# Kernel tuning notes

Hardware: AMD Instinct MI355X
Metric: run time of the kernel (lower is better)

The kernel has to match this reference:

```python
import jax, jax.numpy as jnp
import numpy as np

DECAY = 0.99   # LIF membrane decay
INH = 1.625    # lateral inhibition strength (mode='max')


def setup_inputs() -> dict:
    key = jax.random.key(0)
    kx, kw = jax.random.split(key)
    B, Cin, Cout = 8192, 4096, 1024
    x = (jax.random.uniform(kx, (B, Cin)) < 0.2).astype(jnp.float32)
    # weights, then normweight(): clamp to [0,1] and scale each row so row-max == 0.1
    W = jax.random.uniform(kw, (Cout, Cin), dtype=jnp.float32)
    W = W / (W.max(axis=1, keepdims=True) / 0.1)
    return {"x": x, "W": W, "time_window": 10}


def reference(x, W, time_window):
    # current through the bias-free linear layer; constant across timesteps
    i = x @ W.T                                   # (B, Cout)
    # adaptive threshold init: threshold = 3 * max over batch (thre_init branch)
    thr = 3.0 * i.max(axis=0)                     # (Cout,)
    imax = i.max(axis=1, keepdims=True)           # (B, 1), for mode='max' inhibition
    C = i.shape[1]

    def step(mem, _):
        mem = mem * DECAY + i                     # LIF integration
        s = (mem > thr).astype(i.dtype)           # threshold fire
        mem = mem * (1.0 - s)                     # hard reset at all spikers
        row = s.max(axis=1, keepdims=True)        # (B,1) 1 if any neuron in row spiked
        # winner-take-all k=1: keep a single spiking neuron per row (first/argmax)
        wta = jax.nn.one_hot(jnp.argmax(s, axis=1), C, dtype=i.dtype) * row
        # lateral inhibition: subtract inh * max-current from losers in rows that spiked
        mem = mem - INH * imax * (row - wta)
        return mem, wta

    mem0 = jnp.zeros_like(i)
    _, wtas = jax.lax.scan(step, mem0, None, length=time_window)
    return wtas.sum(axis=0)                       # accumulated spikes (B, Cout)
```

## Files before the change

kernel.cpp:

```cpp
#include <hip/hip_runtime.h>
#include <cstdint>

#define B_DIM 8192
#define CIN   4096
#define COUT  1024

constexpr double W_SCALE   = 83230720.0;
constexpr int    QMAX      = 8323072;
constexpr double INV_SCALE = 0.1 / 8323072.0;

using i32x4 = __attribute__((ext_vector_type(4))) int;

__device__ __forceinline__ void async_copy16(void* lds, const void* g) {
    auto l = (__attribute__((address_space(3))) void*)(uintptr_t)(lds);
    auto p = (const __attribute__((address_space(1))) void*)(uintptr_t)(g);
    __builtin_amdgcn_global_load_lds(p, l, 16, 0, 0);
}

__global__ void prep_x(const float* __restrict__ x, int8_t* __restrict__ Ai) {
    const int idx = blockIdx.x * 256 + threadIdx.x;
    const float4* xp = (const float4*)x + (size_t)idx * 4;
    float4 v0 = xp[0], v1 = xp[1], v2 = xp[2], v3 = xp[3];
    auto pk = [](float a, float b, float c, float d) -> int {
        return (a != 0.f ? 1 : 0) | ((b != 0.f ? 1 : 0) << 8) |
               ((c != 0.f ? 1 : 0) << 16) | ((d != 0.f ? 1 : 0) << 24);
    };
    int4 r;
    r.x = pk(v0.x, v0.y, v0.z, v0.w);
    r.y = pk(v1.x, v1.y, v1.z, v1.w);
    r.z = pk(v2.x, v2.y, v2.z, v2.w);
    r.w = pk(v3.x, v3.y, v3.z, v3.w);
    ((int4*)Ai)[idx] = r;
}

__global__ void prep_w(const float* __restrict__ W, int8_t* __restrict__ Bd,
                       unsigned long long* __restrict__ cm) {
    const int idx = blockIdx.x * 256 + threadIdx.x;
    float4 w = ((const float4*)W)[idx];
    float ws[4] = {w.x, w.y, w.z, w.w};
    char dg[3][4];
#pragma unroll
    for (int k = 0; k < 4; ++k) {
        int qv = __double2int_rn((double)ws[k] * W_SCALE);
        qv = max(0, min(QMAX, qv));
        int d0 = ((qv + 128) & 255) - 128; int tq = (qv - d0) >> 8;
        int d1 = ((tq + 128) & 255) - 128; int d2 = (tq - d1) >> 8;
        dg[0][k] = (char)d0; dg[1][k] = (char)d1; dg[2][k] = (char)d2;
    }
    const size_t off = (size_t)idx * 4;
#pragma unroll
    for (int p = 0; p < 3; ++p) {
        char4 c4; c4.x = dg[p][0]; c4.y = dg[p][1]; c4.z = dg[p][2]; c4.w = dg[p][3];
        *(char4*)(Bd + (size_t)p * COUT * CIN + off) = c4;
    }
    if (idx < COUT) cm[idx] = 0ull;
}

__device__ __forceinline__ void mma16(const i32x4 (&a)[8], const i32x4 (&b)[4],
                                      i32x4 (*accp)[2]) {
    __builtin_amdgcn_s_setprio(1);
#pragma unroll
    for (int kk = 0; kk < 2; ++kk)
#pragma unroll
        for (int mi = 0; mi < 4; ++mi)
#pragma unroll
            for (int ni = 0; ni < 2; ++ni)
                accp[mi][ni] = __builtin_amdgcn_mfma_i32_16x16x64_i8(
                    a[kk * 4 + mi], b[kk * 2 + ni], accp[mi][ni], 0, 0, 0);
    __builtin_amdgcn_s_setprio(0);
}

#define BAR()    __builtin_amdgcn_s_barrier()
#define SCHED0() __builtin_amdgcn_sched_barrier(0)
#define VMW(n)   asm volatile("s_waitcnt vmcnt(" #n ")" ::: "memory")

__global__ __launch_bounds__(256, 2) void gemm_i8(const int8_t* __restrict__ A,
                                                  const int8_t* __restrict__ Bm,
                                                  double* __restrict__ Sc,
                                                  unsigned long long* __restrict__ cm) {
    __shared__ alignas(16) int8_t lds[40960];
    const int tid  = threadIdx.x;
    const int lane = tid & 63;
    const int wave = tid >> 6;

    const int wg = (int)blockIdx.x;
    const int bn = ((wg & 7) << 1) | ((wg >> 3) & 1);
    const int bm = wg >> 4;

    const int stid   = tid >> 3;
    const int cswz16 = ((tid & 7) ^ (stid & 7)) << 4;
    const int8_t* gA = A  + (size_t)(bm * 128 + stid) * CIN + cswz16;
    const int8_t* gB = Bm + (size_t)(bn * 64  + stid) * CIN + cswz16;
    const int wv1024 = wave << 10;

#define SA_(t_) do {                                                            \
    int8_t* d_ = lds + wv1024;                                                  \
    const int8_t* s_ = gA + ((t_) << 7);                                        \
    async_copy16(d_,         s_);                                               \
    async_copy16(d_ + 4096,  s_ + (size_t)32 * CIN);                            \
    async_copy16(d_ + 8192,  s_ + (size_t)64 * CIN);                            \
    async_copy16(d_ + 12288, s_ + (size_t)96 * CIN);                            \
} while (0)
#define SB_(t_, p_) do {                                                        \
    int8_t* d_ = lds + 16384 + ((p_) << 13) + wv1024;                           \
    const int8_t* s_ = gB + (size_t)(p_) * COUT * CIN + ((t_) << 7);            \
    async_copy16(d_,        s_);                                                \
    async_copy16(d_ + 4096, s_ + (size_t)32 * CIN);                             \
} while (0)

    const int wr = wave >> 1, wc = wave & 1;
    const int fr = lane & 15;
    const int q  = lane >> 4;
    const int ck0 = (q ^ (fr & 7)) << 4;
    const int abase = (wr * 64 + fr) * 128;
    const int bbase = 16384 + (wc * 32 + fr) * 128;

    i32x4 a[8], b[4];
    i32x4 acc[3][4][2] = {};

#define LDA_() do {                                                             \
    const int8_t* p_ = lds + abase;                                             \
    _Pragma("unroll")                                                           \
    for (int kk_ = 0; kk_ < 2; ++kk_)                                           \
        _Pragma("unroll")                                                       \
        for (int mi_ = 0; mi_ < 4; ++mi_)                                       \
            a[kk_ * 4 + mi_] = *(const i32x4*)(p_ + mi_ * 2048 + (ck0 ^ (kk_ * 64))); \
} while (0)
#define LDB_(p_) do {                                                           \
    const int8_t* q_ = lds + ((p_) << 13) + bbase;                              \
    _Pragma("unroll")                                                           \
    for (int kk_ = 0; kk_ < 2; ++kk_)                                           \
        _Pragma("unroll")                                                       \
        for (int ni_ = 0; ni_ < 2; ++ni_)                                       \
            b[kk_ * 2 + ni_] = *(const i32x4*)(q_ + ni_ * 2048 + (ck0 ^ (kk_ * 64))); \
} while (0)

    SA_(0); SB_(0, 0); SB_(0, 1);
    VMW(2); BAR(); SCHED0();

#pragma unroll 1
    for (int t = 0; t < 31; ++t) {
        LDA_(); LDB_(0); SB_(t, 2);
        mma16(a, b, acc[0]); VMW(2); BAR(); SCHED0();
        LDB_(1); SA_(t + 1); SB_(t + 1, 0);
        mma16(a, b, acc[1]); VMW(6); BAR(); SCHED0();
        LDB_(2); SB_(t + 1, 1);
        mma16(a, b, acc[2]); VMW(2); BAR(); SCHED0();
    }
    LDA_(); LDB_(0); SB_(31, 2);
    mma16(a, b, acc[0]); VMW(2); BAR(); SCHED0();
    LDB_(1);
    mma16(a, b, acc[1]); VMW(0); BAR(); SCHED0();
    LDB_(2);
    mma16(a, b, acc[2]); BAR();

    const int gm0 = bm * 128 + wr * 64 + q * 4;
    const int gn0 = bn * 64 + wc * 32 + fr;
    double vmax[2] = {0.0, 0.0};
#pragma unroll
    for (int mi = 0; mi < 4; ++mi)
#pragma unroll
        for (int ni = 0; ni < 2; ++ni) {
            const int gn = gn0 + ni * 16;
#pragma unroll
            for (int reg = 0; reg < 4; ++reg) {
                const int gm = gm0 + mi * 16 + reg;
                long long isum = (long long)acc[0][mi][ni][reg]
                               + 256ll   * (long long)acc[1][mi][ni][reg]
                               + 65536ll * (long long)acc[2][mi][ni][reg];
                double v = (double)isum * INV_SCALE;
                Sc[(size_t)gm * COUT + gn] = v;
                vmax[ni] = fmax(vmax[ni], v);
            }
        }
#pragma unroll
    for (int ni = 0; ni < 2; ++ni) {
        vmax[ni] = fmax(vmax[ni], __shfl_xor(vmax[ni], 16, 64));
        vmax[ni] = fmax(vmax[ni], __shfl_xor(vmax[ni], 32, 64));
    }
    double* red = (double*)lds;
    if (lane < 16) {
#pragma unroll
        for (int ni = 0; ni < 2; ++ni)
            red[wave * 32 + ni * 16 + fr] = vmax[ni];
    }
    __syncthreads();
    if (tid < 64) {
        const int c = tid;
        double m = fmax(red[c], red[64 + c]);
        atomicMax(cm + bn * 64 + c, (unsigned long long)__double_as_longlong(m));
    }
#undef SA_
#undef SB_
#undef LDA_
#undef LDB_
}

__global__ void scan_k(const double* __restrict__ Sc, const unsigned long long* __restrict__ cm,
                       const int* __restrict__ twp, float* __restrict__ out) {
    const int lane = threadIdx.x & 63;
    const int wave = threadIdx.x >> 6;
    const int b = blockIdx.x * 4 + wave;
    const int T = *twp;
    const double* row = Sc + (size_t)b * COUT;

    double iv[16], mem[16], thr[16];
    int cnt[16];
    double imax = 0.0;
#pragma unroll
    for (int u = 0; u < 16; ++u) {
        const int j = lane + u * 64;
        iv[u]  = row[j];
        thr[u] = 3.0 * __longlong_as_double((long long)cm[j]);
        mem[u] = 0.0; cnt[u] = 0;
        imax = fmax(imax, iv[u]);
    }
#pragma unroll
    for (int d = 32; d >= 1; d >>= 1) imax = fmax(imax, __shfl_xor(imax, d, 64));
    const double h = 1.625 * imax;

    for (int t = 0; t < T; ++t) {
        int first = 0x7fffffff;
        bool sp[16];
#pragma unroll
        for (int u = 0; u < 16; ++u) {
            mem[u] = mem[u] * 0.99 + iv[u];
            sp[u] = mem[u] > thr[u];
            if (sp[u]) first = min(first, lane + u * 64);
        }
#pragma unroll
        for (int d = 32; d >= 1; d >>= 1) first = min(first, __shfl_xor(first, d, 64));
        const bool rowspike = first < 0x7fffffff;
#pragma unroll
        for (int u = 0; u < 16; ++u) {
            if (sp[u]) mem[u] = 0.0;
            if (rowspike) {
                if (lane + u * 64 == first) cnt[u]++;
                else mem[u] -= h;
            }
        }
    }
#pragma unroll
    for (int u = 0; u < 16; ++u)
        out[(size_t)b * COUT + lane + u * 64] = (float)cnt[u];
}

extern "C" void kernel_launch(void* const* d_in, const int* in_sizes, int n_in,
                              void* d_out, int out_size, void* d_ws, size_t ws_size,
                              hipStream_t stream) {
    const float* x  = (const float*)d_in[0];
    const float* W  = (const float*)d_in[1];
    const int*   tw = (const int*)d_in[2];
    float* out = (float*)d_out;

    int8_t* Ai = (int8_t*)d_ws;
    int8_t* Bd = Ai + (size_t)B_DIM * CIN;
    double* Sc = (double*)(Bd + (size_t)3 * COUT * CIN);
    unsigned long long* cm =
        (unsigned long long*)((int8_t*)Sc + (size_t)B_DIM * COUT * 8);

    hipLaunchKernelGGL(prep_x,  dim3(8192), dim3(256), 0, stream, x, Ai);
    hipLaunchKernelGGL(prep_w,  dim3(4096), dim3(256), 0, stream, W, Bd, cm);
    hipLaunchKernelGGL(gemm_i8, dim3(1024), dim3(256), 0, stream, Ai, Bd, Sc, cm);
    hipLaunchKernelGGL(scan_k,  dim3(2048), dim3(256), 0, stream, Sc, cm, tw, out);
}
```

Baseline: 322.0 us.

## Double-buffer B tiles in int8 GEMM and merge prep kernels into one launch

```diff
diff --git a/kernel.cpp b/kernel.cpp
--- a/kernel.cpp
+++ b/kernel.cpp
@@ -17,43 +17,45 @@
     __builtin_amdgcn_global_load_lds(p, l, 16, 0, 0);
 }
 
-__global__ void prep_x(const float* __restrict__ x, int8_t* __restrict__ Ai) {
-    const int idx = blockIdx.x * 256 + threadIdx.x;
-    const float4* xp = (const float4*)x + (size_t)idx * 4;
-    float4 v0 = xp[0], v1 = xp[1], v2 = xp[2], v3 = xp[3];
-    auto pk = [](float a, float b, float c, float d) -> int {
-        return (a != 0.f ? 1 : 0) | ((b != 0.f ? 1 : 0) << 8) |
-               ((c != 0.f ? 1 : 0) << 16) | ((d != 0.f ? 1 : 0) << 24);
-    };
-    int4 r;
-    r.x = pk(v0.x, v0.y, v0.z, v0.w);
-    r.y = pk(v1.x, v1.y, v1.z, v1.w);
-    r.z = pk(v2.x, v2.y, v2.z, v2.w);
-    r.w = pk(v3.x, v3.y, v3.z, v3.w);
-    ((int4*)Ai)[idx] = r;
-}
-
-__global__ void prep_w(const float* __restrict__ W, int8_t* __restrict__ Bd,
-                       unsigned long long* __restrict__ cm) {
-    const int idx = blockIdx.x * 256 + threadIdx.x;
-    float4 w = ((const float4*)W)[idx];
-    float ws[4] = {w.x, w.y, w.z, w.w};
-    char dg[3][4];
-#pragma unroll
-    for (int k = 0; k < 4; ++k) {
-        int qv = __double2int_rn((double)ws[k] * W_SCALE);
-        qv = max(0, min(QMAX, qv));
-        int d0 = ((qv + 128) & 255) - 128; int tq = (qv - d0) >> 8;
-        int d1 = ((tq + 128) & 255) - 128; int d2 = (tq - d1) >> 8;
-        dg[0][k] = (char)d0; dg[1][k] = (char)d1; dg[2][k] = (char)d2;
-    }
-    const size_t off = (size_t)idx * 4;
-#pragma unroll
-    for (int p = 0; p < 3; ++p) {
-        char4 c4; c4.x = dg[p][0]; c4.y = dg[p][1]; c4.z = dg[p][2]; c4.w = dg[p][3];
-        *(char4*)(Bd + (size_t)p * COUT * CIN + off) = c4;
-    }
-    if (idx < COUT) cm[idx] = 0ull;
+__global__ void prep_xw(const float* __restrict__ x, const float* __restrict__ W,
+                        int8_t* __restrict__ Ai, int8_t* __restrict__ Bd,
+                        unsigned long long* __restrict__ cm) {
+    const int bid = blockIdx.x;
+    if (bid < 8192) {
+        const int idx = bid * 256 + threadIdx.x;
+        const float4* xp = (const float4*)x + (size_t)idx * 4;
+        float4 v0 = xp[0], v1 = xp[1], v2 = xp[2], v3 = xp[3];
+        auto pk = [](float a, float b, float c, float d) -> int {
+            return (a != 0.f ? 1 : 0) | ((b != 0.f ? 1 : 0) << 8) |
+                   ((c != 0.f ? 1 : 0) << 16) | ((d != 0.f ? 1 : 0) << 24);
+        };
+        int4 r;
+        r.x = pk(v0.x, v0.y, v0.z, v0.w);
+        r.y = pk(v1.x, v1.y, v1.z, v1.w);
+        r.z = pk(v2.x, v2.y, v2.z, v2.w);
+        r.w = pk(v3.x, v3.y, v3.z, v3.w);
+        ((int4*)Ai)[idx] = r;
+    } else {
+        const int idx = (bid - 8192) * 256 + threadIdx.x;
+        float4 w = ((const float4*)W)[idx];
+        float ws[4] = {w.x, w.y, w.z, w.w};
+        char dg[3][4];
+#pragma unroll
+        for (int k = 0; k < 4; ++k) {
+            int qv = __double2int_rn((double)ws[k] * W_SCALE);
+            qv = max(0, min(QMAX, qv));
+            int d0 = ((qv + 128) & 255) - 128; int tq = (qv - d0) >> 8;
+            int d1 = ((tq + 128) & 255) - 128; int d2 = (tq - d1) >> 8;
+            dg[0][k] = (char)d0; dg[1][k] = (char)d1; dg[2][k] = (char)d2;
+        }
+        const size_t off = (size_t)idx * 4;
+#pragma unroll
+        for (int p = 0; p < 3; ++p) {
+            char4 c4; c4.x = dg[p][0]; c4.y = dg[p][1]; c4.z = dg[p][2]; c4.w = dg[p][3];
+            *(char4*)(Bd + (size_t)p * COUT * CIN + off) = c4;
+        }
+        if (idx < COUT) cm[idx] = 0ull;
+    }
 }
 
 __device__ __forceinline__ void mma16(const i32x4 (&a)[8], const i32x4 (&b)[4],
@@ -78,7 +80,7 @@
                                                   const int8_t* __restrict__ Bm,
                                                   double* __restrict__ Sc,
                                                   unsigned long long* __restrict__ cm) {
-    __shared__ alignas(16) int8_t lds[40960];
+    __shared__ alignas(16) int8_t lds[65536];
     const int tid  = threadIdx.x;
     const int lane = tid & 63;
     const int wave = tid >> 6;
@@ -101,8 +103,8 @@
     async_copy16(d_ + 8192,  s_ + (size_t)64 * CIN);                            \
     async_copy16(d_ + 12288, s_ + (size_t)96 * CIN);                            \
 } while (0)
-#define SB_(t_, p_) do {                                                        \
-    int8_t* d_ = lds + 16384 + ((p_) << 13) + wv1024;                           \
+#define SB_(t_, p_, db_) do {                                                   \
+    int8_t* d_ = lds + 16384 + ((p_) << 14) + ((db_) << 13) + wv1024;           \
     const int8_t* s_ = gB + (size_t)(p_) * COUT * CIN + ((t_) << 7);            \
     async_copy16(d_,        s_);                                                \
     async_copy16(d_ + 4096, s_ + (size_t)32 * CIN);                             \
@@ -113,9 +115,9 @@
     const int q  = lane >> 4;
     const int ck0 = (q ^ (fr & 7)) << 4;
     const int abase = (wr * 64 + fr) * 128;
-    const int bbase = 16384 + (wc * 32 + fr) * 128;
-
-    i32x4 a[8], b[4];
+    const int bbase = (wc * 32 + fr) * 128;
+
+    i32x4 a[8], bX[4], bY[4];
     i32x4 acc[3][4][2] = {};
 
 #define LDA_() do {                                                             \
@@ -126,33 +128,38 @@
         for (int mi_ = 0; mi_ < 4; ++mi_)                                       \
             a[kk_ * 4 + mi_] = *(const i32x4*)(p_ + mi_ * 2048 + (ck0 ^ (kk_ * 64))); \
 } while (0)
-#define LDB_(p_) do {                                                           \
-    const int8_t* q_ = lds + ((p_) << 13) + bbase;                              \
+#define LDB_(dst_, p_, db_) do {                                                \
+    const int8_t* q_ = lds + 16384 + ((p_) << 14) + ((db_) << 13) + bbase;      \
     _Pragma("unroll")                                                           \
     for (int kk_ = 0; kk_ < 2; ++kk_)                                           \
         _Pragma("unroll")                                                       \
         for (int ni_ = 0; ni_ < 2; ++ni_)                                       \
-            b[kk_ * 2 + ni_] = *(const i32x4*)(q_ + ni_ * 2048 + (ck0 ^ (kk_ * 64))); \
-} while (0)
-
-    SA_(0); SB_(0, 0); SB_(0, 1);
+            dst_[kk_ * 2 + ni_] = *(const i32x4*)(q_ + ni_ * 2048 + (ck0 ^ (kk_ * 64))); \
+} while (0)
+
+#define TILE(t_, dR_, dW_, b0_, b1_)                                            \
+     LDA_(); LDB_(b1_, 1, dR_); SB_((t_) + 1, 0, dW_);                  \
+    SCHED0(); mma16(a, b0_, acc[0]); VMW(2); BAR(); SCHED0();                   \
+     LDB_(b0_, 2, dR_); SA_((t_) + 1); SB_((t_) + 1, 1, dW_);           \
+    SCHED0(); mma16(a, b1_, acc[1]); VMW(6); BAR(); SCHED0();                   \
+     LDB_(b1_, 0, dW_); SB_((t_) + 1, 2, dW_);                          \
+    SCHED0(); mma16(a, b0_, acc[2]); VMW(2); BAR(); SCHED0();
+
+    SA_(0); SB_(0, 0, 0); SB_(0, 1, 0); SB_(0, 2, 0);
     VMW(2); BAR(); SCHED0();
+    LDB_(bX, 0, 0);
 
 #pragma unroll 1
-    for (int t = 0; t < 31; ++t) {
-        LDA_(); LDB_(0); SB_(t, 2);
-        mma16(a, b, acc[0]); VMW(2); BAR(); SCHED0();
-        LDB_(1); SA_(t + 1); SB_(t + 1, 0);
-        mma16(a, b, acc[1]); VMW(6); BAR(); SCHED0();
-        LDB_(2); SB_(t + 1, 1);
-        mma16(a, b, acc[2]); VMW(2); BAR(); SCHED0();
-    }
-    LDA_(); LDB_(0); SB_(31, 2);
-    mma16(a, b, acc[0]); VMW(2); BAR(); SCHED0();
-    LDB_(1);
-    mma16(a, b, acc[1]); VMW(0); BAR(); SCHED0();
-    LDB_(2);
-    mma16(a, b, acc[2]); BAR();
+    for (int t = 0; t < 30; t += 2) {
+        TILE(t,     0, 1, bX, bY)
+        TILE(t + 1, 1, 0, bY, bX)
+    }
+    TILE(30, 0, 1, bX, bY)
+    LDA_(); LDB_(bX, 1, 1);
+    SCHED0(); mma16(a, bY, acc[0]); VMW(0); BAR(); SCHED0();
+    LDB_(bY, 2, 1);
+    SCHED0(); mma16(a, bX, acc[1]); BAR(); SCHED0();
+    SCHED0(); mma16(a, bY, acc[2]); BAR();
 
     const int gm0 = bm * 128 + wr * 64 + q * 4;
     const int gn0 = bn * 64 + wc * 32 + fr;
@@ -194,6 +201,7 @@
 #undef SB_
 #undef LDA_
 #undef LDB_
+#undef TILE
 }
 
 __global__ void scan_k(const double* __restrict__ Sc, const unsigned long long* __restrict__ cm,
@@ -259,8 +267,7 @@
     unsigned long long* cm =
         (unsigned long long*)((int8_t*)Sc + (size_t)B_DIM * COUT * 8);
 
-    hipLaunchKernelGGL(prep_x,  dim3(8192), dim3(256), 0, stream, x, Ai);
-    hipLaunchKernelGGL(prep_w,  dim3(4096), dim3(256), 0, stream, W, Bd, cm);
-    hipLaunchKernelGGL(gemm_i8, dim3(1024), dim3(256), 0, stream, Ai, Bd, Sc, cm);
-    hipLaunchKernelGGL(scan_k,  dim3(2048), dim3(256), 0, stream, Sc, cm, tw, out);
-}
+    hipLaunchKernelGGL(prep_xw, dim3(12288), dim3(256), 0, stream, x, W, Ai, Bd, cm);
+    hipLaunchKernelGGL(gemm_i8, dim3(1024),  dim3(256), 0, stream, Ai, Bd, Sc, cm);
+    hipLaunchKernelGGL(scan_k,  dim3(2048),  dim3(256), 0, stream, Sc, cm, tw, out);
+}
```

New measurement: 325.5 us. About the same (+1.1%).
